# Kernel tuning notes

Measured on AMD Instinct MI355X. Metric: run time of the kernel, lower is better.

## Reference

```python
import jax, jax.numpy as jnp
import numpy as np

N = 100000


def gcn_conv(x, W, b, src, dst, n):
    # PyG GCNConv (default): add self-loops, symmetric normalization,
    # linear transform then scatter-add aggregation.
    h = x @ W  # [N, out_dim]
    # self-loops
    loop = jnp.arange(n, dtype=src.dtype)
    s = jnp.concatenate([src, loop])
    d = jnp.concatenate([dst, loop])
    deg = jnp.zeros((n,), dtype=h.dtype).at[d].add(1.0)
    dinv = jnp.where(deg > 0, jax.lax.rsqrt(deg), 0.0)
    norm = dinv[s] * dinv[d]  # [E+N]
    msg = h[s] * norm[:, None]  # gather + scale
    out = jax.ops.segment_sum(msg, d, num_segments=n)  # scatter-add
    return out + b


def setup_inputs() -> dict:
    key = jax.random.key(0)
    ks = jax.random.split(key, 8)
    in_dim, h_dim, num_classes, E = 128, 128, 16, 800000
    x = jax.random.normal(ks[0], (N, in_dim), dtype=jnp.float32)
    edge_index = jax.random.randint(ks[1], (2, E), 0, N, dtype=jnp.int64)
    s1 = 1.0 / np.sqrt(in_dim)
    s2 = 1.0 / np.sqrt(h_dim)
    W1 = jax.random.uniform(ks[2], (in_dim, h_dim), jnp.float32, -s1, s1)
    b1 = jnp.zeros((h_dim,), jnp.float32)
    W2 = jax.random.uniform(ks[3], (h_dim, h_dim), jnp.float32, -s2, s2)
    b2 = jnp.zeros((h_dim,), jnp.float32)
    Wh = jax.random.uniform(ks[4], (h_dim, num_classes), jnp.float32, -s2, s2)
    bh = jax.random.uniform(ks[5], (num_classes,), jnp.float32, -s2, s2)
    return {"x": x, "W1": W1, "b1": b1, "W2": W2, "b2": b2,
            "Wh": Wh, "bh": bh, "edge_index": edge_index}


def reference(x, W1, b1, W2, b2, Wh, bh, edge_index):
    src, dst = edge_index[0], edge_index[1]
    h = gcn_conv(x, W1, b1, src, dst, N)
    h = jax.nn.relu(h)
    # dropout is identity in eval mode
    h = gcn_conv(h, W2, b2, src, dst, N)
    h = jax.nn.relu(h)
    return h @ Wh + bh  # [N, num_classes]
```

## Files before the change

### kernel.cpp

```cpp
#include <hip/hip_runtime.h>
#include <hip/hip_bf16.h>

typedef short bf16x8 __attribute__((ext_vector_type(8)));
typedef unsigned short u16x8 __attribute__((ext_vector_type(8)));
typedef float f32x4 __attribute__((ext_vector_type(4)));

#define BCAP   64
#define NBINS  256
#define EPB    2048
#define BINCAP 4096

static __device__ __forceinline__ short f2bf(float f) {
    union { float f; unsigned u; } v; v.f = f;
    unsigned r = v.u + 0x7FFF + ((v.u >> 16) & 1);
    return (short)(r >> 16);
}
static __device__ __forceinline__ float bf2f(short h) {
    union { unsigned u; float f; } v;
    v.u = ((unsigned)(unsigned short)h) << 16;
    return v.f;
}
static __device__ __forceinline__ float bfu2f(unsigned short h) {
    union { unsigned u; float f; } v;
    v.u = ((unsigned)h) << 16;
    return v.f;
}
static __device__ __forceinline__ float dinv_of(int deg) {
    return rsqrtf((float)deg + 1.0f);
}


__global__ __launch_bounds__(256) void k_pre(
    int* __restrict__ cursor,
    const float* __restrict__ W1, short* __restrict__ b1hi, short* __restrict__ b1lo,
    const float* __restrict__ W2, short* __restrict__ b2hi, short* __restrict__ b2lo) {
    const int b = blockIdx.x;
    const int t = threadIdx.x;
    if (b == 0) {
        if (t < NBINS / 4) *(int4*)(cursor + t * 4) = make_int4(0, 0, 0, 0);
        return;
    }
    int wb = b - 1;
    const float* W = (wb < 8) ? W1 : W2;
    short* BH = (wb < 8) ? b1hi : b2hi;
    short* BL = (wb < 8) ? b1lo : b2lo;
    int u = (wb & 7) * 256 + t;
    int nb = u >> 8, k8 = (u >> 4) & 15, c16 = u & 15;
    int col = nb * 16 + c16, k0 = k8 * 8;
    bf16x8 h, l;
    #pragma unroll
    for (int j = 0; j < 8; ++j) {
        float v = W[(size_t)(k0 + j) * 128 + col];
        short hh = f2bf(v);
        h[j] = hh;
        l[j] = f2bf(v - bf2f(hh));
    }
    *(bf16x8*)(BH + (size_t)u * 8) = h;
    *(bf16x8*)(BL + (size_t)u * 8) = l;
}


template <bool F32A, bool SCALE>
static __device__ __forceinline__ void gemm_core(
    unsigned short* As,
    const void* __restrict__ Aptr,
    const short* __restrict__ Bp_hi, const short* __restrict__ Bp_lo,
    const int* __restrict__ indeg, unsigned short* __restrict__ Cbf,
    int M, int bid) {
    const int tid  = threadIdx.x;
    const int wave = tid >> 6;
    const int lane = tid & 63;
    const int r16  = lane & 15;
    const int kg   = lane >> 4;
    const int m0   = bid * 128;
    const int mh   = (wave >> 1) * 64;
    const int nb0  = (wave & 1) * 4;

    #pragma unroll
    for (int rr = 0; rr < 8; ++rr) {
        int u = rr * 256 + tid;
        int row = u >> 4, c = u & 15;
        int rowg = m0 + row;
        if (rowg >= M) rowg = M - 1;
        bf16x8 v;
        if (F32A) {
            const float* ap = (const float*)Aptr + (size_t)rowg * 128 + c * 8;
            float4 a0 = *(const float4*)ap;
            float4 a1 = *(const float4*)(ap + 4);
            v[0] = f2bf(a0.x); v[1] = f2bf(a0.y); v[2] = f2bf(a0.z); v[3] = f2bf(a0.w);
            v[4] = f2bf(a1.x); v[5] = f2bf(a1.y); v[6] = f2bf(a1.z); v[7] = f2bf(a1.w);
        } else {
            v = *(const bf16x8*)((const unsigned short*)Aptr + (size_t)rowg * 128 + c * 8);
        }
        *(bf16x8*)(As + (size_t)(row * 16 + (c ^ (row & 7))) * 8) = v;
    }

    bf16x8 bufh[2][4], bufl[2][4];
    #pragma unroll
    for (int ni = 0; ni < 4; ++ni) {
        size_t uB = (size_t)(nb0 + ni) * 256 + (size_t)kg * 16 + r16;
        bufh[0][ni] = *(const bf16x8*)(Bp_hi + uB * 8);
        bufl[0][ni] = *(const bf16x8*)(Bp_lo + uB * 8);
    }

    __syncthreads();

    f32x4 acc[4][4] = {};

    #pragma unroll
    for (int ks = 0; ks < 4; ++ks) {
        const int cur = ks & 1, nxt = cur ^ 1;
        if (ks < 3) {
            #pragma unroll
            for (int ni = 0; ni < 4; ++ni) {
                size_t uB = (size_t)(nb0 + ni) * 256 + (size_t)((ks + 1) * 4 + kg) * 16 + r16;
                bufh[nxt][ni] = *(const bf16x8*)(Bp_hi + uB * 8);
                bufl[nxt][ni] = *(const bf16x8*)(Bp_lo + uB * 8);
            }
        }
        bf16x8 a[4];
        const int c = ks * 4 + kg;
        #pragma unroll
        for (int mi = 0; mi < 4; ++mi) {
            int row = mh + mi * 16 + r16;
            a[mi] = *(const bf16x8*)(As + (size_t)(row * 16 + (c ^ (row & 7))) * 8);
        }
        #pragma unroll
        for (int mi = 0; mi < 4; ++mi)
            #pragma unroll
            for (int ni = 0; ni < 4; ++ni) {
                acc[mi][ni] = __builtin_amdgcn_mfma_f32_16x16x32_bf16(a[mi], bufl[cur][ni], acc[mi][ni], 0, 0, 0);
                acc[mi][ni] = __builtin_amdgcn_mfma_f32_16x16x32_bf16(a[mi], bufh[cur][ni], acc[mi][ni], 0, 0, 0);
            }
    }

    const int n0 = (wave & 1) * 64;
    #pragma unroll
    for (int mi = 0; mi < 4; ++mi) {
        #pragma unroll
        for (int r = 0; r < 4; ++r) {
            int row = m0 + mh + mi * 16 + (lane >> 4) * 4 + r;
            if (row < M) {
                float dr = SCALE ? dinv_of(indeg[row]) : 1.0f;
                #pragma unroll
                for (int ni = 0; ni < 4; ++ni) {
                    int col = n0 + ni * 16 + r16;
                    Cbf[(size_t)row * 128 + col] = (unsigned short)f2bf(acc[mi][ni][r] * dr);
                }
            }
        }
    }
}


__global__ __launch_bounds__(256) void k_gemm1_partA(
    const float* __restrict__ X,
    const short* __restrict__ Bp_hi, const short* __restrict__ Bp_lo,
    unsigned short* __restrict__ Cbf, int M,
    int cblocks, int total,
    const int* __restrict__ srcv, const int* __restrict__ dstv,
    int* __restrict__ cursor, int2* __restrict__ partSD,
    int E, int N) {
    __shared__ unsigned short As[128 * 128];
    const int b = blockIdx.x;
    const int lo = (int)((long long)b * cblocks / total);
    const int hi = (int)(((long long)b + 1) * cblocks / total);
    if (hi > lo) {
        int*  S       = (int*)As;
        int*  hist    = S;
        int*  incl    = S + 256;
        int*  basePos = S + 512;
        int2* stage   = (int2*)(S + 1024);
        const int t = threadIdx.x;
        hist[t] = 0;
        __syncthreads();

        const int ebase = lo * EPB + t;
        int pk[8], sv[8], dv[8];
        #pragma unroll
        for (int r = 0; r < 8; ++r) {
            int e = ebase + r * 256;
            pk[r] = -1;
            if (e < E) {
                sv[r] = srcv[e];
                dv[r] = dstv[e];
                int bin = (dv[r] * NBINS) / N;
                int rank = atomicAdd(&hist[bin], 1);
                pk[r] = (bin << 12) | rank;
            }
        }
        __syncthreads();

        const int h = hist[t];
        incl[t] = h;
        __syncthreads();
        #pragma unroll
        for (int off = 1; off < 256; off <<= 1) {
            int x = (t >= off) ? incl[t - off] : 0;
            __syncthreads();
            incl[t] += x;
            __syncthreads();
        }
        basePos[t] = atomicAdd(&cursor[t], h);
        hist[t] = incl[t] - h;
        __syncthreads();

        #pragma unroll
        for (int r = 0; r < 8; ++r) {
            if (pk[r] >= 0) {
                int bin = pk[r] >> 12;
                stage[hist[bin] + (pk[r] & 4095)] = make_int2(sv[r], dv[r]);
            }
        }
        __syncthreads();

        const int count = incl[255];
        for (int j = t; j < count; j += 256) {
            int2 sd = stage[j];
            int bin = (sd.y * NBINS) / N;
            int pos = basePos[bin] + (j - hist[bin]);
            if (pos < BINCAP) partSD[(size_t)bin * BINCAP + pos] = sd;
        }
        return;
    }
    gemm_core<true, false>(As, X, Bp_hi, Bp_lo, nullptr, Cbf, M, b - lo);
}


__global__ __launch_bounds__(256) void k_partB(
    const int2* __restrict__ partSD, const int* __restrict__ cursor,
    int* __restrict__ bucket, int* __restrict__ indeg, int N) {
    __shared__ int cnt[400];
    const int b = blockIdx.x;
    const int t = threadIdx.x;
    const int n0 = (b * N + NBINS - 1) / NBINS;
    const int n1 = ((b + 1) * N + NBINS - 1) / NBINS;
    const int range = n1 - n0;
    for (int i = t; i < range; i += 256) cnt[i] = 0;
    __syncthreads();
    const int m = min(cursor[b], BINCAP);
    const size_t base = (size_t)b * BINCAP;
    for (int j = t; j < m; j += 256) {
        int2 sd = partSD[base + j];
        int r = atomicAdd(&cnt[sd.y - n0], 1);
        if (r < BCAP) bucket[(size_t)sd.y * BCAP + r] = sd.x;
    }
    __syncthreads();
    for (int i = t; i < range; i += 256) indeg[n0 + i] = cnt[i];
}

__global__ __launch_bounds__(256) void k_gemm_mfma(
    const unsigned short* __restrict__ Abf,
    const short* __restrict__ Bp_hi, const short* __restrict__ Bp_lo,
    const int* __restrict__ indeg, unsigned short* __restrict__ Cbf, int M) {
    __shared__ unsigned short As[128 * 128];
    gemm_core<false, true>(As, Abf, Bp_hi, Bp_lo, indeg, Cbf, M, blockIdx.x);
}


template <bool EDGEDINV>
__global__ __launch_bounds__(256) void k_aggregate(const unsigned short* __restrict__ hp,
                                                   const int* __restrict__ bucket,
                                                   const int* __restrict__ indeg,
                                                   const float* __restrict__ bias,
                                                   unsigned short* __restrict__ outBf, int n) {
    const int wave = (blockIdx.x * 256 + threadIdx.x) >> 6;
    const int sub  = (threadIdx.x >> 4) & 3;
    const int l16  = threadIdx.x & 15;
    const int i    = wave * 4 + sub;
    if (i >= n) return;

    const u16x8* __restrict__ h8 = (const u16x8*)hp;
    const int deg0 = indeg[i];
    const int deg  = (deg0 < BCAP) ? deg0 : BCAP;
    const float di = dinv_of(deg0);
    const int* __restrict__ blist = bucket + (size_t)i * BCAP;

    u16x8 sv = h8[(size_t)i * 16 + l16];
    float a[8], b[8];
    #pragma unroll
    for (int q = 0; q < 8; ++q) {
        a[q] = EDGEDINV ? bfu2f(sv[q]) * di : bfu2f(sv[q]);
        b[q] = 0.f;
    }

    int j = 0;
    while (j < deg) {
        const int e1 = deg - 1;
        int   idx[8];
        float m[8];
        #pragma unroll
        for (int t = 0; t < 8; ++t) {
            int jt = j + t;
            bool ct = jt < deg;
            idx[t] = blist[ct ? jt : e1];
            m[t] = ct ? 1.f : 0.f;
        }
        if (EDGEDINV) {
            #pragma unroll
            for (int t = 0; t < 8; ++t) m[t] *= dinv_of(indeg[idx[t]]);
        }
        u16x8 v[8];
        #pragma unroll
        for (int t = 0; t < 8; ++t) v[t] = h8[(size_t)idx[t] * 16 + l16];
        #pragma unroll
        for (int t = 0; t < 8; t += 2) {
            #pragma unroll
            for (int q = 0; q < 8; ++q) {
                a[q] = fmaf(bfu2f(v[t][q]),     m[t],     a[q]);
                b[q] = fmaf(bfu2f(v[t + 1][q]), m[t + 1], b[q]);
            }
        }
        j += 8;
    }

    float4 bs0 = ((const float4*)bias)[l16 * 2];
    float4 bs1 = ((const float4*)bias)[l16 * 2 + 1];
    float bb[8] = {bs0.x, bs0.y, bs0.z, bs0.w, bs1.x, bs1.y, bs1.z, bs1.w};
    u16x8 ov;
    #pragma unroll
    for (int q = 0; q < 8; ++q) {
        float r = fmaxf(fmaf(a[q] + b[q], di, bb[q]), 0.f);
        ov[q] = (unsigned short)f2bf(r);
    }
    ((u16x8*)outBf)[(size_t)i * 16 + l16] = ov;
}


__global__ __launch_bounds__(256) void k_gemm_head(const unsigned short* __restrict__ A,
                                                   const float* __restrict__ Wh,
                                                   const float* __restrict__ bh,
                                                   float* __restrict__ C, int M) {
    __shared__ float Ws[128 * 16];
    const int t = threadIdx.x;
    *(float4*)&Ws[t * 8]     = *(const float4*)&Wh[t * 8];
    *(float4*)&Ws[t * 8 + 4] = *(const float4*)&Wh[t * 8 + 4];
    __syncthreads();

    const int wave = t >> 6;
    const int lane = t & 63;
    const int r    = lane & 15;
    const int kq   = lane >> 4;
    int row = (blockIdx.x * 4 + wave) * 16 + r;
    int lrow = (row < M) ? row : (M - 1);

    const u16x8* ap = (const u16x8*)(A + (size_t)lrow * 128 + kq * 32);
    float acc[16] = {};
    #pragma unroll
    for (int k8 = 0; k8 < 4; ++k8) {
        u16x8 av = ap[k8];
        #pragma unroll
        for (int q = 0; q < 8; ++q) {
            int k = kq * 32 + k8 * 8 + q;
            float aval = bfu2f(av[q]);
            #pragma unroll
            for (int c = 0; c < 16; ++c)
                acc[c] = fmaf(aval, Ws[k * 16 + c], acc[c]);
        }
    }
    #pragma unroll
    for (int c = 0; c < 16; ++c) {
        acc[c] += __shfl_down(acc[c], 16);
        acc[c] += __shfl_down(acc[c], 32);
    }
    if (lane < 16 && row < M) {
        float* orow = C + (size_t)row * 16;
        #pragma unroll
        for (int c = 0; c < 16; c += 4) {
            float4 v = make_float4(acc[c] + bh[c], acc[c + 1] + bh[c + 1],
                                   acc[c + 2] + bh[c + 2], acc[c + 3] + bh[c + 3]);
            *(float4*)(orow + c) = v;
        }
    }
}


extern "C" void kernel_launch(void* const* d_in, const int* in_sizes, int n_in,
                              void* d_out, int out_size, void* d_ws, size_t ws_size,
                              hipStream_t stream) {
    const float* x  = (const float*)d_in[0];
    const float* W1 = (const float*)d_in[1];
    const float* b1 = (const float*)d_in[2];
    const float* W2 = (const float*)d_in[3];
    const float* b2 = (const float*)d_in[4];
    const float* Wh = (const float*)d_in[5];
    const float* bh = (const float*)d_in[6];
    const int*   ei = (const int*)d_in[7];

    const int N = in_sizes[0] / 128;
    const int E = in_sizes[7] / 2;
    const int* src = ei;
    const int* dst = ei + E;
    float* out = (float*)d_out;

    char* w = (char*)d_ws;
    auto alloc = [&](size_t bytes) -> void* {
        void* p = (void*)w;
        w += (bytes + 255) & ~(size_t)255;
        return p;
    };
    unsigned short* hp     = (unsigned short*)alloc((size_t)N * 128 * sizeof(short));
    unsigned short* actB   = (unsigned short*)alloc((size_t)N * 128 * sizeof(short));
    int*   indeg  = (int*)alloc((size_t)N * sizeof(int));
    int*   bucket = (int*)alloc((size_t)N * BCAP * sizeof(int));
    int*   cursor = (int*)alloc((size_t)NBINS * sizeof(int));
    int2*  partSD = (int2*)alloc((size_t)NBINS * BINCAP * sizeof(int2));
    short* w1hiP  = (short*)alloc(128 * 128 * sizeof(short));
    short* w1loP  = (short*)alloc(128 * 128 * sizeof(short));
    short* w2hiP  = (short*)alloc(128 * 128 * sizeof(short));
    short* w2loP  = (short*)alloc(128 * 128 * sizeof(short));

    const int gblocks = (N + 127) / 128;
    const int ablocks = (N + 15) / 16;
    const int cblocks = (E + EPB - 1) / EPB;
    const int total   = gblocks + cblocks;

    k_pre<<<17, 256, 0, stream>>>(cursor, W1, w1hiP, w1loP, W2, w2hiP, w2loP);
    k_gemm1_partA<<<total, 256, 0, stream>>>(x, w1hiP, w1loP, hp, N,
                                             cblocks, total, src, dst,
                                             cursor, partSD, E, N);
    k_partB<<<NBINS, 256, 0, stream>>>(partSD, cursor, bucket, indeg, N);
    k_aggregate<true><<<ablocks, 256, 0, stream>>>(hp, bucket, indeg, b1, actB, N);
    k_gemm_mfma<<<gblocks, 256, 0, stream>>>(actB, w2hiP, w2loP, indeg, hp, N);
    k_aggregate<false><<<ablocks, 256, 0, stream>>>(hp, bucket, indeg, b2, actB, N);
    k_gemm_head<<<(N + 63) / 64, 256, 0, stream>>>(actB, Wh, bh, out, N);
}
```

Measured before the change: 155.9 us.

## Aggregate before second GEMM and fuse GEMM2 with MFMA head

Reorders layer two so the propagation runs on the 128-wide activations before the W2 transform, using linearity, then fuses GEMM2, bias, ReLU and the classifier head into one MFMA kernel that keeps the intermediate tile in shared memory. It also precomputes per-node inverse sqrt degrees once in the partition kernel and shrinks the aggregation gather batch from 8 to 4 edges. The aim is to drop one full N×128 bf16 write and read plus a kernel launch, and to replace repeated rsqrt and indeg lookups with a single table load. Reordering changes where bf16 rounding happens, which may shift numerical results slightly.

Result: faster. 132.9 us, median of 2 (-14.7%).

```diff
diff --git a/kernel.cpp b/kernel.cpp
--- a/kernel.cpp
+++ b/kernel.cpp
@@ -25,19 +25,31 @@
     v.u = ((unsigned)h) << 16;
     return v.f;
 }
-static __device__ __forceinline__ float dinv_of(int deg) {
-    return rsqrtf((float)deg + 1.0f);
-}
 
 
 __global__ __launch_bounds__(256) void k_pre(
     int* __restrict__ cursor,
     const float* __restrict__ W1, short* __restrict__ b1hi, short* __restrict__ b1lo,
-    const float* __restrict__ W2, short* __restrict__ b2hi, short* __restrict__ b2lo) {
+    const float* __restrict__ W2, short* __restrict__ b2hi, short* __restrict__ b2lo,
+    const float* __restrict__ Wh, short* __restrict__ whhi, short* __restrict__ whlo) {
     const int b = blockIdx.x;
     const int t = threadIdx.x;
     if (b == 0) {
         if (t < NBINS / 4) *(int4*)(cursor + t * 4) = make_int4(0, 0, 0, 0);
+        return;
+    }
+    if (b == 17) {
+        int k8 = t >> 4, c16 = t & 15, k0 = k8 * 8;
+        bf16x8 h, l;
+        #pragma unroll
+        for (int j = 0; j < 8; ++j) {
+            float v = Wh[(size_t)(k0 + j) * 16 + c16];
+            short hh = f2bf(v);
+            h[j] = hh;
+            l[j] = f2bf(v - bf2f(hh));
+        }
+        *(bf16x8*)(whhi + (size_t)t * 8) = h;
+        *(bf16x8*)(whlo + (size_t)t * 8) = l;
         return;
     }
     int wb = b - 1;
@@ -60,19 +72,16 @@
 }
 
 
-template <bool F32A, bool SCALE>
-static __device__ __forceinline__ void gemm_core(
-    unsigned short* As,
-    const void* __restrict__ Aptr,
+template <bool F32A>
+static __device__ __forceinline__ void gemm_tile_acc(
+    unsigned short* As, const void* __restrict__ Aptr,
     const short* __restrict__ Bp_hi, const short* __restrict__ Bp_lo,
-    const int* __restrict__ indeg, unsigned short* __restrict__ Cbf,
-    int M, int bid) {
+    int M, int m0, f32x4 (&acc)[4][4]) {
     const int tid  = threadIdx.x;
     const int wave = tid >> 6;
     const int lane = tid & 63;
     const int r16  = lane & 15;
     const int kg   = lane >> 4;
-    const int m0   = bid * 128;
     const int mh   = (wave >> 1) * 64;
     const int nb0  = (wave & 1) * 4;
 
@@ -105,8 +114,6 @@
 
     __syncthreads();
 
-    f32x4 acc[4][4] = {};
-
     #pragma unroll
     for (int ks = 0; ks < 4; ++ks) {
         const int cur = ks & 1, nxt = cur ^ 1;
@@ -132,23 +139,6 @@
                 acc[mi][ni] = __builtin_amdgcn_mfma_f32_16x16x32_bf16(a[mi], bufl[cur][ni], acc[mi][ni], 0, 0, 0);
                 acc[mi][ni] = __builtin_amdgcn_mfma_f32_16x16x32_bf16(a[mi], bufh[cur][ni], acc[mi][ni], 0, 0, 0);
             }
-    }
-
-    const int n0 = (wave & 1) * 64;
-    #pragma unroll
-    for (int mi = 0; mi < 4; ++mi) {
-        #pragma unroll
-        for (int r = 0; r < 4; ++r) {
-            int row = m0 + mh + mi * 16 + (lane >> 4) * 4 + r;
-            if (row < M) {
-                float dr = SCALE ? dinv_of(indeg[row]) : 1.0f;
-                #pragma unroll
-                for (int ni = 0; ni < 4; ++ni) {
-                    int col = n0 + ni * 16 + r16;
-                    Cbf[(size_t)row * 128 + col] = (unsigned short)f2bf(acc[mi][ni][r] * dr);
-                }
-            }
-        }
     }
 }
 
@@ -223,13 +213,35 @@
         }
         return;
     }
-    gemm_core<true, false>(As, X, Bp_hi, Bp_lo, nullptr, Cbf, M, b - lo);
+
+    f32x4 acc[4][4] = {};
+    gemm_tile_acc<true>(As, X, Bp_hi, Bp_lo, M, (b - lo) * 128, acc);
+
+    const int lane = threadIdx.x & 63;
+    const int wave = threadIdx.x >> 6;
+    const int r16  = lane & 15;
+    const int m0   = (b - lo) * 128;
+    const int mh   = (wave >> 1) * 64;
+    const int n0   = (wave & 1) * 64;
+    #pragma unroll
+    for (int mi = 0; mi < 4; ++mi)
+        #pragma unroll
+        for (int r = 0; r < 4; ++r) {
+            int row = m0 + mh + mi * 16 + (lane >> 4) * 4 + r;
+            if (row < M) {
+                #pragma unroll
+                for (int ni = 0; ni < 4; ++ni)
+                    Cbf[(size_t)row * 128 + n0 + ni * 16 + r16] =
+                        (unsigned short)f2bf(acc[mi][ni][r]);
+            }
+        }
 }
 
 
 __global__ __launch_bounds__(256) void k_partB(
     const int2* __restrict__ partSD, const int* __restrict__ cursor,
-    int* __restrict__ bucket, int* __restrict__ indeg, int N) {
+    int* __restrict__ bucket, int* __restrict__ indeg, float* __restrict__ dinvA,
+    int N) {
     __shared__ int cnt[400];
     const int b = blockIdx.x;
     const int t = threadIdx.x;
@@ -246,22 +258,18 @@
         if (r < BCAP) bucket[(size_t)sd.y * BCAP + r] = sd.x;
     }
     __syncthreads();
-    for (int i = t; i < range; i += 256) indeg[n0 + i] = cnt[i];
-}
-
-__global__ __launch_bounds__(256) void k_gemm_mfma(
-    const unsigned short* __restrict__ Abf,
-    const short* __restrict__ Bp_hi, const short* __restrict__ Bp_lo,
-    const int* __restrict__ indeg, unsigned short* __restrict__ Cbf, int M) {
-    __shared__ unsigned short As[128 * 128];
-    gemm_core<false, true>(As, Abf, Bp_hi, Bp_lo, indeg, Cbf, M, blockIdx.x);
-}
-
-
-template <bool EDGEDINV>
+    for (int i = t; i < range; i += 256) {
+        indeg[n0 + i] = cnt[i];
+        dinvA[n0 + i] = rsqrtf((float)cnt[i] + 1.0f);
+    }
+}
+
+
+template <bool EDGEDINV, bool FINISH>
 __global__ __launch_bounds__(256) void k_aggregate(const unsigned short* __restrict__ hp,
                                                    const int* __restrict__ bucket,
                                                    const int* __restrict__ indeg,
+                                                   const float* __restrict__ dinvA,
                                                    const float* __restrict__ bias,
                                                    unsigned short* __restrict__ outBf, int n) {
     const int wave = (blockIdx.x * 256 + threadIdx.x) >> 6;
@@ -273,7 +281,7 @@
     const u16x8* __restrict__ h8 = (const u16x8*)hp;
     const int deg0 = indeg[i];
     const int deg  = (deg0 < BCAP) ? deg0 : BCAP;
-    const float di = dinv_of(deg0);
+    const float di = dinvA[i];
     const int* __restrict__ blist = bucket + (size_t)i * BCAP;
 
     u16x8 sv = h8[(size_t)i * 16 + l16];
@@ -287,10 +295,10 @@
     int j = 0;
     while (j < deg) {
         const int e1 = deg - 1;
-        int   idx[8];
-        float m[8];
-        #pragma unroll
-        for (int t = 0; t < 8; ++t) {
+        int   idx[4];
+        float m[4];
+        #pragma unroll
+        for (int t = 0; t < 4; ++t) {
             int jt = j + t;
             bool ct = jt < deg;
             idx[t] = blist[ct ? jt : e1];
@@ -298,78 +306,99 @@
         }
         if (EDGEDINV) {
             #pragma unroll
-            for (int t = 0; t < 8; ++t) m[t] *= dinv_of(indeg[idx[t]]);
-        }
-        u16x8 v[8];
-        #pragma unroll
-        for (int t = 0; t < 8; ++t) v[t] = h8[(size_t)idx[t] * 16 + l16];
-        #pragma unroll
-        for (int t = 0; t < 8; t += 2) {
+            for (int t = 0; t < 4; ++t) m[t] *= dinvA[idx[t]];
+        }
+        u16x8 v[4];
+        #pragma unroll
+        for (int t = 0; t < 4; ++t) v[t] = h8[(size_t)idx[t] * 16 + l16];
+        #pragma unroll
+        for (int t = 0; t < 4; t += 2) {
             #pragma unroll
             for (int q = 0; q < 8; ++q) {
                 a[q] = fmaf(bfu2f(v[t][q]),     m[t],     a[q]);
                 b[q] = fmaf(bfu2f(v[t + 1][q]), m[t + 1], b[q]);
             }
         }
-        j += 8;
-    }
-
-    float4 bs0 = ((const float4*)bias)[l16 * 2];
-    float4 bs1 = ((const float4*)bias)[l16 * 2 + 1];
-    float bb[8] = {bs0.x, bs0.y, bs0.z, bs0.w, bs1.x, bs1.y, bs1.z, bs1.w};
+        j += 4;
+    }
+
     u16x8 ov;
-    #pragma unroll
-    for (int q = 0; q < 8; ++q) {
-        float r = fmaxf(fmaf(a[q] + b[q], di, bb[q]), 0.f);
-        ov[q] = (unsigned short)f2bf(r);
+    if (FINISH) {
+        float4 bs0 = ((const float4*)bias)[l16 * 2];
+        float4 bs1 = ((const float4*)bias)[l16 * 2 + 1];
+        float bb[8] = {bs0.x, bs0.y, bs0.z, bs0.w, bs1.x, bs1.y, bs1.z, bs1.w};
+        #pragma unroll
+        for (int q = 0; q < 8; ++q) {
+            float r = fmaxf(fmaf(a[q] + b[q], di, bb[q]), 0.f);
+            ov[q] = (unsigned short)f2bf(r * di);
+        }
+    } else {
+        #pragma unroll
+        for (int q = 0; q < 8; ++q)
+            ov[q] = (unsigned short)f2bf((a[q] + b[q]) * di);
     }
     ((u16x8*)outBf)[(size_t)i * 16 + l16] = ov;
 }
 
 
-__global__ __launch_bounds__(256) void k_gemm_head(const unsigned short* __restrict__ A,
-                                                   const float* __restrict__ Wh,
-                                                   const float* __restrict__ bh,
-                                                   float* __restrict__ C, int M) {
-    __shared__ float Ws[128 * 16];
-    const int t = threadIdx.x;
-    *(float4*)&Ws[t * 8]     = *(const float4*)&Wh[t * 8];
-    *(float4*)&Ws[t * 8 + 4] = *(const float4*)&Wh[t * 8 + 4];
+__global__ __launch_bounds__(256) void k_gemm2_head(
+    const unsigned short* __restrict__ T,
+    const short* __restrict__ B2hi, const short* __restrict__ B2lo,
+    const float* __restrict__ b2,
+    const short* __restrict__ whhi, const short* __restrict__ whlo,
+    const float* __restrict__ bh,
+    float* __restrict__ out, int M) {
+    __shared__ unsigned short As[128 * 128];
+    const int tid  = threadIdx.x;
+    const int wave = tid >> 6;
+    const int lane = tid & 63;
+    const int r16  = lane & 15;
+    const int kg   = lane >> 4;
+    const int m0   = blockIdx.x * 128;
+    const int mh   = (wave >> 1) * 64;
+    const int n0   = (wave & 1) * 64;
+
+    f32x4 acc[4][4] = {};
+    gemm_tile_acc<false>(As, T, B2hi, B2lo, M, m0, acc);
+
     __syncthreads();
 
-    const int wave = t >> 6;
-    const int lane = t & 63;
-    const int r    = lane & 15;
-    const int kq   = lane >> 4;
-    int row = (blockIdx.x * 4 + wave) * 16 + r;
-    int lrow = (row < M) ? row : (M - 1);
-
-    const u16x8* ap = (const u16x8*)(A + (size_t)lrow * 128 + kq * 32);
-    float acc[16] = {};
-    #pragma unroll
-    for (int k8 = 0; k8 < 4; ++k8) {
-        u16x8 av = ap[k8];
-        #pragma unroll
-        for (int q = 0; q < 8; ++q) {
-            int k = kq * 32 + k8 * 8 + q;
-            float aval = bfu2f(av[q]);
+    float b2v[4];
+    #pragma unroll
+    for (int ni = 0; ni < 4; ++ni) b2v[ni] = b2[n0 + ni * 16 + r16];
+    #pragma unroll
+    for (int mi = 0; mi < 4; ++mi)
+        #pragma unroll
+        for (int r = 0; r < 4; ++r) {
+            int rowl = mh + mi * 16 + (lane >> 4) * 4 + r;
             #pragma unroll
-            for (int c = 0; c < 16; ++c)
-                acc[c] = fmaf(aval, Ws[k * 16 + c], acc[c]);
-        }
-    }
-    #pragma unroll
-    for (int c = 0; c < 16; ++c) {
-        acc[c] += __shfl_down(acc[c], 16);
-        acc[c] += __shfl_down(acc[c], 32);
-    }
-    if (lane < 16 && row < M) {
-        float* orow = C + (size_t)row * 16;
-        #pragma unroll
-        for (int c = 0; c < 16; c += 4) {
-            float4 v = make_float4(acc[c] + bh[c], acc[c + 1] + bh[c + 1],
-                                   acc[c + 2] + bh[c + 2], acc[c + 3] + bh[c + 3]);
-            *(float4*)(orow + c) = v;
+            for (int ni = 0; ni < 4; ++ni) {
+                int col = n0 + ni * 16 + r16;
+                float u = fmaxf(acc[mi][ni][r] + b2v[ni], 0.f);
+                As[(size_t)(rowl * 16 + ((col >> 3) ^ (rowl & 7))) * 8 + (col & 7)] =
+                    (unsigned short)f2bf(u);
+            }
+        }
+    __syncthreads();
+
+    const float bhv = bh[r16];
+    #pragma unroll
+    for (int mt2 = 0; mt2 < 2; ++mt2) {
+        const int mt = wave * 2 + mt2;
+        f32x4 acc2 = {};
+        #pragma unroll
+        for (int ks = 0; ks < 4; ++ks) {
+            const int c = ks * 4 + kg;
+            const int row = mt * 16 + r16;
+            bf16x8 a = *(const bf16x8*)(As + (size_t)(row * 16 + (c ^ (row & 7))) * 8);
+            size_t uB = (size_t)(ks * 4 + kg) * 16 + r16;
+            acc2 = __builtin_amdgcn_mfma_f32_16x16x32_bf16(a, *(const bf16x8*)(whlo + uB * 8), acc2, 0, 0, 0);
+            acc2 = __builtin_amdgcn_mfma_f32_16x16x32_bf16(a, *(const bf16x8*)(whhi + uB * 8), acc2, 0, 0, 0);
+        }
+        #pragma unroll
+        for (int r = 0; r < 4; ++r) {
+            int row = m0 + mt * 16 + (lane >> 4) * 4 + r;
+            if (row < M) out[(size_t)row * 16 + r16] = acc2[r] + bhv;
         }
     }
 }
@@ -402,6 +431,7 @@
     unsigned short* hp     = (unsigned short*)alloc((size_t)N * 128 * sizeof(short));
     unsigned short* actB   = (unsigned short*)alloc((size_t)N * 128 * sizeof(short));
     int*   indeg  = (int*)alloc((size_t)N * sizeof(int));
+    float* dinvA  = (float*)alloc((size_t)N * sizeof(float));
     int*   bucket = (int*)alloc((size_t)N * BCAP * sizeof(int));
     int*   cursor = (int*)alloc((size_t)NBINS * sizeof(int));
     int2*  partSD = (int2*)alloc((size_t)NBINS * BINCAP * sizeof(int2));
@@ -409,19 +439,24 @@
     short* w1loP  = (short*)alloc(128 * 128 * sizeof(short));
     short* w2hiP  = (short*)alloc(128 * 128 * sizeof(short));
     short* w2loP  = (short*)alloc(128 * 128 * sizeof(short));
+    short* whhiP  = (short*)alloc(128 * 16 * sizeof(short));
+    short* whloP  = (short*)alloc(128 * 16 * sizeof(short));
 
     const int gblocks = (N + 127) / 128;
     const int ablocks = (N + 15) / 16;
     const int cblocks = (E + EPB - 1) / EPB;
     const int total   = gblocks + cblocks;
 
-    k_pre<<<17, 256, 0, stream>>>(cursor, W1, w1hiP, w1loP, W2, w2hiP, w2loP);
+    k_pre<<<18, 256, 0, stream>>>(cursor, W1, w1hiP, w1loP, W2, w2hiP, w2loP,
+                                  Wh, whhiP, whloP);
     k_gemm1_partA<<<total, 256, 0, stream>>>(x, w1hiP, w1loP, hp, N,
                                              cblocks, total, src, dst,
                                              cursor, partSD, E, N);
-    k_partB<<<NBINS, 256, 0, stream>>>(partSD, cursor, bucket, indeg, N);
-    k_aggregate<true><<<ablocks, 256, 0, stream>>>(hp, bucket, indeg, b1, actB, N);
-    k_gemm_mfma<<<gblocks, 256, 0, stream>>>(actB, w2hiP, w2loP, indeg, hp, N);
-    k_aggregate<false><<<ablocks, 256, 0, stream>>>(hp, bucket, indeg, b2, actB, N);
-    k_gemm_head<<<(N + 63) / 64, 256, 0, stream>>>(actB, Wh, bh, out, N);
-}
+    k_partB<<<NBINS, 256, 0, stream>>>(partSD, cursor, bucket, indeg, dinvA, N);
+    k_aggregate<true, true><<<ablocks, 256, 0, stream>>>(hp, bucket, indeg, dinvA,
+                                                         b1, actB, N);
+    k_aggregate<false, false><<<ablocks, 256, 0, stream>>>(actB, bucket, indeg, dinvA,
+                                                           nullptr, hp, N);
+    k_gemm2_head<<<gblocks, 256, 0, stream>>>(hp, w2hiP, w2loP, b2,
+                                              whhiP, whloP, bh, out, N);
+}
```
